# Optimization experiments

Hardware: AMD Instinct MI355X
Metric: run time of the kernel (lower is better)

The kernel has to match this reference:

```python
import math
import jax, jax.numpy as jnp
import numpy as np

V, D, H, F, L = 32128, 768, 12, 3072, 12
NUM_BUCKETS, MAX_DIST = 32, 128
B, S = 16, 512
EPS = 1e-6


def _rel_bucket(rel_pos, num_buckets=NUM_BUCKETS, max_distance=MAX_DIST):
    # bidirectional T5 bucketing
    num_buckets //= 2
    ret = (rel_pos > 0).astype(jnp.int32) * num_buckets
    n = jnp.abs(rel_pos)
    max_exact = num_buckets // 2
    is_small = n < max_exact
    large = max_exact + (
        jnp.log(n.astype(jnp.float32) / max_exact)
        / math.log(max_distance / max_exact)
        * (num_buckets - max_exact)
    ).astype(jnp.int32)
    large = jnp.minimum(large, num_buckets - 1)
    return ret + jnp.where(is_small, n.astype(jnp.int32), large)


def t5_layernorm(x, w):
    # RMS norm: no mean subtraction, no bias
    var = jnp.mean(x * x, axis=-1, keepdims=True)
    return x * jax.lax.rsqrt(var + EPS) * w


def setup_inputs() -> dict:
    key = jax.random.key(0)
    ks = jax.random.split(key, 12)
    sc = 0.02
    inp = {
        "tokens": jax.random.randint(ks[0], (B, S), 0, V, dtype=jnp.int64),
        "emb": jax.random.normal(ks[1], (V, D), jnp.float32) * sc,
        "rel_bias": jax.random.normal(ks[2], (NUM_BUCKETS, H), jnp.float32) * sc,
        "ln1_w": jnp.ones((L, D), jnp.float32),
        "wq": jax.random.normal(ks[3], (L, D, D), jnp.float32) * sc,
        "wk": jax.random.normal(ks[4], (L, D, D), jnp.float32) * sc,
        "wv": jax.random.normal(ks[5], (L, D, D), jnp.float32) * sc,
        "wo": jax.random.normal(ks[6], (L, D, D), jnp.float32) * sc,
        "ln2_w": jnp.ones((L, D), jnp.float32),
        "w1": jax.random.normal(ks[7], (L, D, F), jnp.float32) * sc,
        "w2": jax.random.normal(ks[8], (L, F, D), jnp.float32) * sc,
        "ln_final_w": jnp.ones((D,), jnp.float32),
    }
    return inp


def _attn(x, pos_bias, wq, wk, wv, wo):
    b, s, d = x.shape
    dh = d // H
    q = (x @ wq).reshape(b, s, H, dh).transpose(0, 2, 1, 3)
    k = (x @ wk).reshape(b, s, H, dh).transpose(0, 2, 1, 3)
    v = (x @ wv).reshape(b, s, H, dh).transpose(0, 2, 1, 3)
    # T5: NO 1/sqrt(dh) scaling; add bucketed relative-position bias
    scores = jnp.einsum("bhqd,bhkd->bhqk", q, k) + pos_bias[None]  # [B,H,S,S]
    a = jax.nn.softmax(scores, axis=-1)
    o = jnp.einsum("bhqk,bhkd->bhqd", a, v)
    o = o.transpose(0, 2, 1, 3).reshape(b, s, d)
    return o @ wo


def reference(tokens, emb, rel_bias, ln1_w, wq, wk, wv, wo, ln2_w, w1, w2, ln_final_w):
    x = emb[tokens]  # [B,S,D]
    s = tokens.shape[1]
    pos = jnp.arange(s)
    buckets = _rel_bucket(pos[None, :] - pos[:, None])  # [S,S]
    pos_bias = rel_bias[buckets].transpose(2, 0, 1)  # [H,S,S], computed once (layer 0)
    for i in range(L):
        h = t5_layernorm(x, ln1_w[i])
        x = x + _attn(h, pos_bias, wq[i], wk[i], wv[i], wo[i])
        h = t5_layernorm(x, ln2_w[i])
        x = x + jax.nn.relu(h @ w1[i]) @ w2[i]
    return t5_layernorm(x, ln_final_w)
```

## Files before the change

kernel.cpp:

```cpp
#include <hip/hip_runtime.h>
#include <hip/hip_bf16.h>

typedef unsigned short u16;
typedef unsigned int   u32;
typedef __attribute__((ext_vector_type(8))) __bf16 bf16x8;
typedef __attribute__((ext_vector_type(4))) float  f32x4;
typedef __attribute__((ext_vector_type(4))) u16    u16x4;

#define SEQ     512
#define DMODEL  768
#define NHEAD   12
#define DHEAD   64
#define FDIM    3072
#define NLAYER  12
#define NROWS   8192
#define QKVN    2304

__device__ __forceinline__ u16 f2bf(float f) {
  union { float f; u32 u; } x; x.f = f;
  u32 r = x.u + 0x7fffu + ((x.u >> 16) & 1u);
  return (u16)(r >> 16);
}

__global__ __launch_bounds__(256) void k_transpose_cvt(const float* __restrict__ in,
                                                       u16* __restrict__ out, int K, int N,
                                                       size_t istride, size_t ostride) {
  __shared__ float tile[32][33];
  in  += (size_t)blockIdx.z * istride;
  out += (size_t)blockIdx.z * ostride;
  int nb = blockIdx.x * 32, kb = blockIdx.y * 32;
  int tx = threadIdx.x, ty = threadIdx.y;
#pragma unroll
  for (int i = 0; i < 4; i++)
    tile[ty + 8 * i][tx] = in[(size_t)(kb + ty + 8 * i) * N + nb + tx];
  __syncthreads();
#pragma unroll
  for (int i = 0; i < 4; i++)
    out[(size_t)(nb + ty + 8 * i) * K + kb + tx] = f2bf(tile[tx][ty + 8 * i]);
}

__global__ __launch_bounds__(256) void k_embed(const int* __restrict__ tokens,
                                               const float* __restrict__ emb,
                                               float* __restrict__ x) {
  int idx = blockIdx.x * 256 + threadIdx.x;
  int row = idx / 192, c4 = idx % 192;
  int tok = tokens[row];
  reinterpret_cast<float4*>(x + (size_t)row * DMODEL)[c4] =
      reinterpret_cast<const float4*>(emb + (size_t)tok * DMODEL)[c4];
}

__global__ __launch_bounds__(256) void k_biaslut(const float* __restrict__ rel_bias,
                                                 float* __restrict__ lut) {
  int idx = blockIdx.x * 256 + threadIdx.x;
  int h = idx >> 10, i = idx & 1023;
  int rel = i - 511;
  int ret = rel > 0 ? 16 : 0;
  int n = rel < 0 ? -rel : rel;
  int b;
  if (n < 8) {
    b = n;
  } else {
    float r = logf((float)n * 0.125f) / 2.772588722239781f * 8.0f;
    int lg = 8 + (int)r;
    b = lg < 15 ? lg : 15;
  }
  b += ret;
  lut[idx] = rel_bias[b * NHEAD + h];
}

template <int BF16OUT>
__global__ __launch_bounds__(256) void k_rmsnorm(const float* __restrict__ x,
                                                 const float* __restrict__ w,
                                                 void* __restrict__ out) {
  int row = blockIdx.x * 4 + (threadIdx.x >> 6);
  int lane = threadIdx.x & 63;
  const float4* xr = reinterpret_cast<const float4*>(x + (size_t)row * DMODEL);
  float4 a = xr[lane], b = xr[lane + 64], c = xr[lane + 128];
  float ss = a.x * a.x + a.y * a.y + a.z * a.z + a.w * a.w
           + b.x * b.x + b.y * b.y + b.z * b.z + b.w * b.w
           + c.x * c.x + c.y * c.y + c.z * c.z + c.w * c.w;
#pragma unroll
  for (int off = 1; off < 64; off <<= 1) ss += __shfl_xor(ss, off);
  float sc = rsqrtf(ss * (1.0f / 768.0f) + 1e-6f);
  const float4* wr = reinterpret_cast<const float4*>(w);
  float4 w0 = wr[lane], w1 = wr[lane + 64], w2 = wr[lane + 128];
  if (BF16OUT) {
    u16x4* o = reinterpret_cast<u16x4*>((u16*)out + (size_t)row * DMODEL);
    u16x4 v0, v1, v2;
    v0[0] = f2bf(a.x * sc * w0.x); v0[1] = f2bf(a.y * sc * w0.y);
    v0[2] = f2bf(a.z * sc * w0.z); v0[3] = f2bf(a.w * sc * w0.w);
    v1[0] = f2bf(b.x * sc * w1.x); v1[1] = f2bf(b.y * sc * w1.y);
    v1[2] = f2bf(b.z * sc * w1.z); v1[3] = f2bf(b.w * sc * w1.w);
    v2[0] = f2bf(c.x * sc * w2.x); v2[1] = f2bf(c.y * sc * w2.y);
    v2[2] = f2bf(c.z * sc * w2.z); v2[3] = f2bf(c.w * sc * w2.w);
    o[lane] = v0; o[lane + 64] = v1; o[lane + 128] = v2;
  } else {
    float4* o = reinterpret_cast<float4*>((float*)out + (size_t)row * DMODEL);
    float4 v0, v1, v2;
    v0.x = a.x * sc * w0.x; v0.y = a.y * sc * w0.y; v0.z = a.z * sc * w0.z; v0.w = a.w * sc * w0.w;
    v1.x = b.x * sc * w1.x; v1.y = b.y * sc * w1.y; v1.z = b.z * sc * w1.z; v1.w = b.w * sc * w1.w;
    v2.x = c.x * sc * w2.x; v2.y = c.y * sc * w2.y; v2.z = c.z * sc * w2.z; v2.w = c.w * sc * w2.w;
    o[lane] = v0; o[lane + 64] = v1; o[lane + 128] = v2;
  }
}

__device__ __forceinline__ void gload_lds16(const void* g, void* l) {
  __builtin_amdgcn_global_load_lds((const __attribute__((address_space(1))) void*)g,
                                   (__attribute__((address_space(3))) void*)l, 16, 0, 0);
}

template <int EPI, int NF>
__global__ __launch_bounds__(512, 2) void k_gemm(const u16* __restrict__ A, const u16* __restrict__ Bt,
                                                 u16* __restrict__ outb, float* __restrict__ outf,
                                                 int M, int N, int K) {
  __shared__ u16 lds[3 * 24576];
  const int NT = K >> 6;
  const int BROWS = 2 * NF * 16;
  int tid = threadIdx.x;
  int lane = tid & 63, wid = tid >> 6;
  int lr = lane & 15, lh = lane >> 4;
  int wm = wid >> 1, wn = wid & 1;

  int gx = gridDim.x, gm = gridDim.y;
  int nwg = gx * gm;
  int linear = blockIdx.y * gx + blockIdx.x;
  int cpx = nwg >> 3;
  int swz = (linear & 7) * cpx + (linear >> 3);
  int bn = (swz % gx) * BROWS;
  int bm = (swz / gx) * 256;

  const u16* Ab = A  + (size_t)bm * K;
  const u16* Bb = Bt + (size_t)bn * K;

  f32x4 acc[4][NF] = {};

  auto STAGE_A = [&](int kt, u16* buf) {
#pragma unroll
    for (int i = 0; i < 4; i++) {
      int elem = i * 512 + tid;
      int row = elem >> 3, ch = elem & 7;
      int chs = ch ^ (row & 7);
      gload_lds16(Ab + (size_t)row * K + kt * 64 + chs * 8, buf + elem * 8);
    }
  };
  auto STAGE_B = [&](int kt, u16* buf) {
#pragma unroll
    for (int i = 0; i < 2; i++) {
      int elem = i * 512 + tid;
      int row = elem >> 3, ch = elem & 7;
      if (row >= BROWS) row = BROWS - 1;
      int chs = ch ^ (row & 7);
      gload_lds16(Bb + (size_t)row * K + kt * 64 + chs * 8, buf + 16384 + elem * 8);
    }
  };

  STAGE_A(0, lds);
  STAGE_B(0, lds);
  STAGE_A(1, lds + 24576);
  STAGE_B(1, lds + 24576);
  asm volatile("s_waitcnt vmcnt(6)" ::: "memory");
  __builtin_amdgcn_s_barrier();

  bf16x8 af[4], bfr[2][NF];

#define DSA(KK)                                                                 \
  _Pragma("unroll") for (int i = 0; i < 4; i++) {                               \
    int r = wm * 64 + i * 16 + lr;                                              \
    af[i] = *reinterpret_cast<const bf16x8*>(cur + r * 64 + ((((KK) * 4 + lh) ^ (r & 7)) * 8)); \
  }
#define MFMA_G(KK)                                                              \
  __builtin_amdgcn_s_setprio(1);                                                \
  _Pragma("unroll") for (int i = 0; i < 4; i++)                                 \
  _Pragma("unroll") for (int n = 0; n < NF; n++)                                \
    acc[i][n] = __builtin_amdgcn_mfma_f32_16x16x32_bf16(af[i], bfr[KK][n], acc[i][n], 0, 0, 0); \
  __builtin_amdgcn_s_setprio(0);
#define BAR_LGKM                                                                \
  __builtin_amdgcn_s_barrier();                                                 \
  asm volatile("s_waitcnt lgkmcnt(0)" ::: "memory");                            \
  __builtin_amdgcn_sched_barrier(0);

  int cs = 0;
  for (int t = 0; t < NT; ++t) {
    const u16* cur = lds + cs * 24576;
    int ds = cs + 2; if (ds >= 3) ds -= 3;
    u16* dst = lds + ds * 24576;
    int t2 = t + 2; if (t2 >= NT) t2 -= NT;

#pragma unroll
    for (int kk = 0; kk < 2; kk++)
#pragma unroll
      for (int n = 0; n < NF; n++) {
        int r = wn * (NF * 16) + n * 16 + lr;
        bfr[kk][n] = *reinterpret_cast<const bf16x8*>(cur + 16384 + r * 64 + (((kk * 4 + lh) ^ (r & 7)) * 8));
      }
    DSA(0)
    STAGE_A(t2, dst);
    BAR_LGKM
    MFMA_G(0)
    __builtin_amdgcn_s_barrier();

    DSA(1)
    STAGE_B(t2, dst);
    BAR_LGKM
    MFMA_G(1)
    asm volatile("s_waitcnt vmcnt(6)" ::: "memory");
    __builtin_amdgcn_s_barrier();

    cs += 1; if (cs >= 3) cs -= 3;
  }
#undef DSA
#undef MFMA_G
#undef BAR_LGKM

#pragma unroll
  for (int i = 0; i < 4; i++)
#pragma unroll
    for (int n = 0; n < NF; n++)
#pragma unroll
      for (int r = 0; r < 4; r++) {
        int row = bm + wm * 64 + i * 16 + lh * 4 + r;
        int col = bn + wn * (NF * 16) + n * 16 + lr;
        size_t idx = (size_t)row * N + col;
        float v = acc[i][n][r];
        if (EPI == 0)      outb[idx] = f2bf(v);
        else if (EPI == 1) outb[idx] = f2bf(v > 0.f ? v : 0.f);
        else               outf[idx] += v;
      }
}

__global__ __launch_bounds__(256) void k_vtrans(const u16* __restrict__ qkv, u16* __restrict__ vt) {
  __shared__ u16 t[32][33];
  int bh = blockIdx.z;
  int b = bh / NHEAD, h = bh % NHEAD;
  int d0 = blockIdx.x * 32, s0 = blockIdx.y * 32;
  int tx = threadIdx.x, ty = threadIdx.y;
  const u16* src = qkv + (size_t)(b * SEQ + s0) * QKVN + 2 * DMODEL + h * DHEAD + d0;
#pragma unroll
  for (int i = 0; i < 4; i++)
    t[ty + 8 * i][tx] = src[(size_t)(ty + 8 * i) * QKVN + tx];
  __syncthreads();
  u16* dst = vt + ((size_t)bh * DHEAD + d0) * SEQ + s0;
#pragma unroll
  for (int i = 0; i < 4; i++)
    dst[(size_t)(ty + 8 * i) * SEQ + tx] = t[tx][ty + 8 * i];
}

__global__ __launch_bounds__(256) void k_attn(const u16* __restrict__ qkv,
                                              const u16* __restrict__ vt,
                                              const float* __restrict__ lutg,
                                              u16* __restrict__ ob) {
  __shared__ __align__(16) float lut[1024];
  __shared__ __align__(16) u16 Ks[2][4096];
  __shared__ __align__(16) u16 Vs[2][4096];
  __shared__ __align__(16) u16 Ps[4][2048];
  int b = blockIdx.x / NHEAD, h = blockIdx.x % NHEAD;
  int qt = blockIdx.y;
  int tid = threadIdx.x;
  int lane = tid & 63, wid = tid >> 6;
  int lr = lane & 15, lh = lane >> 4;
  int q0 = qt * 128 + wid * 32;

  reinterpret_cast<float4*>(lut)[tid] = reinterpret_cast<const float4*>(lutg + h * 1024)[tid];

  bf16x8 aq[2][2];
#pragma unroll
  for (int m = 0; m < 2; m++) {
    const u16* qp = qkv + (size_t)(b * SEQ + q0 + m * 16 + lr) * QKVN + h * DHEAD;
#pragma unroll
    for (int kk = 0; kk < 2; kk++)
      aq[m][kk] = *reinterpret_cast<const bf16x8*>(qp + kk * 32 + lh * 8);
  }

  float mrun[2][4], lpart[2][4];
  f32x4 acc_o[2][4] = {};
#pragma unroll
  for (int m = 0; m < 2; m++)
#pragma unroll
    for (int r = 0; r < 4; r++) { mrun[m][r] = -3.0e38f; lpart[m][r] = 0.f; }

  int srow = tid >> 3, sc8 = tid & 7;
  int scs = (sc8 ^ (srow & 7)) << 3;
  const u16* kbase = qkv + (size_t)(b * SEQ + srow) * QKVN + DMODEL + h * DHEAD + scs;
  const u16* vbase = vt + ((size_t)blockIdx.x * DHEAD + srow) * SEQ + scs;

  auto STAGE = [&](int kt, int bufi) {
    int kv0 = kt << 6;
    gload_lds16(kbase + (size_t)kv0 * QKVN,        &Ks[bufi][tid * 8]);
    gload_lds16(kbase + (size_t)(kv0 + 32) * QKVN, &Ks[bufi][2048 + tid * 8]);
    gload_lds16(vbase + kv0,                       &Vs[bufi][tid * 8]);
    gload_lds16(vbase + 32 * SEQ + kv0,            &Vs[bufi][2048 + tid * 8]);
  };

  STAGE(0, 0);
  asm volatile("s_waitcnt vmcnt(0) lgkmcnt(0)" ::: "memory");
  __builtin_amdgcn_s_barrier();

  int ibase = 511 + lr - q0 - lh * 4;
  u16* pw = Ps[wid];

  for (int kt = 0; kt < 8; kt++) {
    int cb = kt & 1;
    __builtin_amdgcn_s_barrier();
    STAGE((kt + 1) & 7, cb ^ 1);
    asm volatile("s_waitcnt vmcnt(4)" ::: "memory");
    __builtin_amdgcn_s_barrier();

    const u16* KsC = Ks[cb];
    const u16* VsC = Vs[cb];
    int kv0 = kt << 6;

    f32x4 sc[2][4] = {};
#pragma unroll
    for (int kk = 0; kk < 2; kk++) {
      bf16x8 bk[4];
#pragma unroll
      for (int n = 0; n < 4; n++) {
        int row = n * 16 + lr;
        int c = (kk * 4 + lh) ^ (lr & 7);
        bk[n] = *reinterpret_cast<const bf16x8*>(KsC + row * 64 + c * 8);
      }
#pragma unroll
      for (int m = 0; m < 2; m++)
#pragma unroll
        for (int n = 0; n < 4; n++)
          sc[m][n] = __builtin_amdgcn_mfma_f32_16x16x32_bf16(aq[m][kk], bk[n], sc[m][n], 0, 0, 0);
    }

    int pred = 1;
    float vmax[2][4];
#pragma unroll
    for (int m = 0; m < 2; m++)
#pragma unroll
      for (int r = 0; r < 4; r++) {
        int ib = ibase + kv0 - m * 16 - r;
#pragma unroll
        for (int n = 0; n < 4; n++)
          sc[m][n][r] += lut[ib + n * 16];
        float v = fmaxf(fmaxf(sc[m][0][r], sc[m][1][r]), fmaxf(sc[m][2][r], sc[m][3][r]));
        v = fmaxf(v, __shfl_xor(v, 1));
        v = fmaxf(v, __shfl_xor(v, 2));
        v = fmaxf(v, __shfl_xor(v, 4));
        v = fmaxf(v, __shfl_xor(v, 8));
        vmax[m][r] = v;
        pred = pred && (v <= mrun[m][r] + 8.0f);
      }
    if (!__all(pred)) {
#pragma unroll
      for (int m = 0; m < 2; m++)
#pragma unroll
        for (int r = 0; r < 4; r++) {
          float mo = mrun[m][r];
          float mn = fmaxf(mo, vmax[m][r]);
          float corr = __expf(mo - mn);
          mrun[m][r] = mn;
          lpart[m][r] *= corr;
#pragma unroll
          for (int n = 0; n < 4; n++) acc_o[m][n][r] *= corr;
        }
    }
#pragma unroll
    for (int m = 0; m < 2; m++)
#pragma unroll
      for (int r = 0; r < 4; r++) {
        float mm = mrun[m][r];
        int prow = m * 16 + lh * 4 + r;
        int pbse = prow * 64;
        int sw = prow & 7;
        float lp = lpart[m][r];
#pragma unroll
        for (int n = 0; n < 4; n++) {
          float pv = __expf(sc[m][n][r] - mm);
          lp += pv;
          pw[pbse + ((((n << 1) | (lr >> 3)) ^ sw) << 3) + (lr & 7)] = f2bf(pv);
        }
        lpart[m][r] = lp;
      }

    asm volatile("s_waitcnt lgkmcnt(0)" ::: "memory");
    __builtin_amdgcn_sched_barrier(0);
#pragma unroll
    for (int kk = 0; kk < 2; kk++) {
      bf16x8 bvv[4], ap[2];
#pragma unroll
      for (int n = 0; n < 4; n++) {
        int row = n * 16 + lr;
        int c = (kk * 4 + lh) ^ (lr & 7);
        bvv[n] = *reinterpret_cast<const bf16x8*>(VsC + row * 64 + c * 8);
      }
#pragma unroll
      for (int m = 0; m < 2; m++) {
        int row = m * 16 + lr;
        int c = (kk * 4 + lh) ^ (lr & 7);
        ap[m] = *reinterpret_cast<const bf16x8*>(pw + row * 64 + c * 8);
      }
#pragma unroll
      for (int m = 0; m < 2; m++)
#pragma unroll
        for (int n = 0; n < 4; n++)
          acc_o[m][n] = __builtin_amdgcn_mfma_f32_16x16x32_bf16(ap[m], bvv[n], acc_o[m][n], 0, 0, 0);
    }
  }

#pragma unroll
  for (int m = 0; m < 2; m++)
#pragma unroll
    for (int r = 0; r < 4; r++) {
      float l = lpart[m][r];
      l += __shfl_xor(l, 1);
      l += __shfl_xor(l, 2);
      l += __shfl_xor(l, 4);
      l += __shfl_xor(l, 8);
      float inv = 1.f / l;
      size_t orow = (size_t)(b * SEQ + q0 + m * 16 + lh * 4 + r);
#pragma unroll
      for (int n = 0; n < 4; n++)
        ob[orow * DMODEL + h * DHEAD + n * 16 + lr] = f2bf(acc_o[m][n][r] * inv);
    }
}

extern "C" void kernel_launch(void* const* d_in, const int* in_sizes, int n_in,
                              void* d_out, int out_size, void* d_ws, size_t ws_size,
                              hipStream_t stream) {
  const int*   tokens = (const int*)  d_in[0];
  const float* emb    = (const float*)d_in[1];
  const float* relb   = (const float*)d_in[2];
  const float* ln1w   = (const float*)d_in[3];
  const float* wq     = (const float*)d_in[4];
  const float* wk     = (const float*)d_in[5];
  const float* wv     = (const float*)d_in[6];
  const float* wo     = (const float*)d_in[7];
  const float* ln2w   = (const float*)d_in[8];
  const float* w1     = (const float*)d_in[9];
  const float* w2     = (const float*)d_in[10];
  const float* lnfw   = (const float*)d_in[11];
  float* out = (float*)d_out;

  char* p = (char*)d_ws;
  auto carve = [&](size_t bytes) { char* r = p; p += (bytes + 255) & ~(size_t)255; return r; };
  const size_t DD = (size_t)DMODEL * DMODEL, DF = (size_t)DMODEL * FDIM;

  u16*   wqkv_t = (u16*)carve(NLAYER * 3 * DD * 2);
  u16*   wo_t   = (u16*)carve(NLAYER * DD * 2);
  u16*   w1_t   = (u16*)carve(NLAYER * DF * 2);
  u16*   w2_t   = (u16*)carve(NLAYER * DF * 2);
  float* x      = (float*)carve((size_t)NROWS * DMODEL * 4);
  u16*   hbuf   = (u16*)carve((size_t)NROWS * DMODEL * 2);
  u16*   qkvbuf = (u16*)carve((size_t)NROWS * QKVN * 2);
  u16*   abuf   = (u16*)carve((size_t)NROWS * DMODEL * 2);
  u16*   fbuf   = (u16*)carve((size_t)NROWS * FDIM * 2);
  float* lutbuf = (float*)carve((size_t)NHEAD * 1024 * 4);
  u16*   vtbuf  = fbuf;

  dim3 tb(32, 8);
  k_transpose_cvt<<<dim3(24, 24, NLAYER), tb, 0, stream>>>(wq, wqkv_t,          DMODEL, DMODEL, DD, 3 * DD);
  k_transpose_cvt<<<dim3(24, 24, NLAYER), tb, 0, stream>>>(wk, wqkv_t + DD,     DMODEL, DMODEL, DD, 3 * DD);
  k_transpose_cvt<<<dim3(24, 24, NLAYER), tb, 0, stream>>>(wv, wqkv_t + 2 * DD, DMODEL, DMODEL, DD, 3 * DD);
  k_transpose_cvt<<<dim3(24, 24, NLAYER), tb, 0, stream>>>(wo, wo_t,            DMODEL, DMODEL, DD, DD);
  k_transpose_cvt<<<dim3(96, 24, NLAYER), tb, 0, stream>>>(w1, w1_t,            DMODEL, FDIM,   DF, DF);
  k_transpose_cvt<<<dim3(24, 96, NLAYER), tb, 0, stream>>>(w2, w2_t,            FDIM, DMODEL,   DF, DF);

  k_embed<<<NROWS * 192 / 256, 256, 0, stream>>>(tokens, emb, x);
  k_biaslut<<<48, 256, 0, stream>>>(relb, lutbuf);

  for (int i = 0; i < NLAYER; i++) {
    k_rmsnorm<1><<<NROWS / 4, 256, 0, stream>>>(x, ln1w + i * DMODEL, hbuf);
    k_gemm<0, 3><<<dim3(24, 32), 512, 0, stream>>>(hbuf, wqkv_t + (size_t)i * 3 * DD, qkvbuf, nullptr,
                                                   NROWS, QKVN, DMODEL);
    k_vtrans<<<dim3(2, 16, 192), tb, 0, stream>>>(qkvbuf, vtbuf);
    k_attn<<<dim3(192, 4), 256, 0, stream>>>(qkvbuf, vtbuf, lutbuf, abuf);
    k_gemm<2, 3><<<dim3(8, 32),  512, 0, stream>>>(abuf, wo_t + (size_t)i * DD, nullptr, x,
                                                   NROWS, DMODEL, DMODEL);
    k_rmsnorm<1><<<NROWS / 4, 256, 0, stream>>>(x, ln2w + i * DMODEL, hbuf);
    k_gemm<1, 4><<<dim3(24, 32), 512, 0, stream>>>(hbuf, w1_t + (size_t)i * DF, fbuf, nullptr,
                                                   NROWS, FDIM, DMODEL);
    k_gemm<2, 3><<<dim3(8, 32),  512, 0, stream>>>(fbuf, w2_t + (size_t)i * DF, nullptr, x,
                                                   NROWS, DMODEL, FDIM);
  }
  k_rmsnorm<0><<<NROWS / 4, 256, 0, stream>>>(x, lnfw, out);
}
```

Before: 3.127 ms.

## Shrink GEMM tiles to 128x96 with 256 threads and double buffering

The GEMM kernel moves from 256-row tiles with 512 threads and a 3-stage LDS ring to 128x96 tiles with 256 threads and a 2-buffer ping-pong. It also drops the NF template parameter, so the FFN up-projection now uses 96-column tiles like the other GEMMs. Grids double in the M dimension to give more workgroups, smaller LDS per block and possibly higher occupancy. The cost is less operand reuse per tile and a full vmcnt(0) wait every iteration, which leaves less global-load latency hidden.

```diff
diff --git a/kernel.cpp b/kernel.cpp
--- a/kernel.cpp
+++ b/kernel.cpp
@@ -109,13 +109,12 @@
                                    (__attribute__((address_space(3))) void*)l, 16, 0, 0);
 }
 
-template <int EPI, int NF>
-__global__ __launch_bounds__(512, 2) void k_gemm(const u16* __restrict__ A, const u16* __restrict__ Bt,
+template <int EPI>
+__global__ __launch_bounds__(256, 2) void k_gemm(const u16* __restrict__ A, const u16* __restrict__ Bt,
                                                  u16* __restrict__ outb, float* __restrict__ outf,
                                                  int M, int N, int K) {
-  __shared__ u16 lds[3 * 24576];
+  __shared__ u16 lds[2 * 14336];
   const int NT = K >> 6;
-  const int BROWS = 2 * NF * 16;
   int tid = threadIdx.x;
   int lane = tid & 63, wid = tid >> 6;
   int lr = lane & 15, lh = lane >> 4;
@@ -126,18 +125,18 @@
   int linear = blockIdx.y * gx + blockIdx.x;
   int cpx = nwg >> 3;
   int swz = (linear & 7) * cpx + (linear >> 3);
-  int bn = (swz % gx) * BROWS;
-  int bm = (swz / gx) * 256;
+  int bn = (swz % gx) * 96;
+  int bm = (swz / gx) * 128;
 
   const u16* Ab = A  + (size_t)bm * K;
   const u16* Bb = Bt + (size_t)bn * K;
 
-  f32x4 acc[4][NF] = {};
+  f32x4 acc[4][3] = {};
 
   auto STAGE_A = [&](int kt, u16* buf) {
 #pragma unroll
     for (int i = 0; i < 4; i++) {
-      int elem = i * 512 + tid;
+      int elem = i * 256 + tid;
       int row = elem >> 3, ch = elem & 7;
       int chs = ch ^ (row & 7);
       gload_lds16(Ab + (size_t)row * K + kt * 64 + chs * 8, buf + elem * 8);
@@ -145,23 +144,20 @@
   };
   auto STAGE_B = [&](int kt, u16* buf) {
 #pragma unroll
-    for (int i = 0; i < 2; i++) {
-      int elem = i * 512 + tid;
+    for (int i = 0; i < 3; i++) {
+      int elem = i * 256 + tid;
       int row = elem >> 3, ch = elem & 7;
-      if (row >= BROWS) row = BROWS - 1;
       int chs = ch ^ (row & 7);
-      gload_lds16(Bb + (size_t)row * K + kt * 64 + chs * 8, buf + 16384 + elem * 8);
+      gload_lds16(Bb + (size_t)row * K + kt * 64 + chs * 8, buf + 8192 + elem * 8);
     }
   };
 
   STAGE_A(0, lds);
   STAGE_B(0, lds);
-  STAGE_A(1, lds + 24576);
-  STAGE_B(1, lds + 24576);
-  asm volatile("s_waitcnt vmcnt(6)" ::: "memory");
+  asm volatile("s_waitcnt vmcnt(0)" ::: "memory");
   __builtin_amdgcn_s_barrier();
 
-  bf16x8 af[4], bfr[2][NF];
+  bf16x8 af[4], bfr[2][3];
 
 #define DSA(KK)                                                                 \
   _Pragma("unroll") for (int i = 0; i < 4; i++) {                               \
@@ -171,7 +167,7 @@
 #define MFMA_G(KK)                                                              \
   __builtin_amdgcn_s_setprio(1);                                                \
   _Pragma("unroll") for (int i = 0; i < 4; i++)                                 \
-  _Pragma("unroll") for (int n = 0; n < NF; n++)                                \
+  _Pragma("unroll") for (int n = 0; n < 3; n++)                                 \
     acc[i][n] = __builtin_amdgcn_mfma_f32_16x16x32_bf16(af[i], bfr[KK][n], acc[i][n], 0, 0, 0); \
   __builtin_amdgcn_s_setprio(0);
 #define BAR_LGKM                                                                \
@@ -179,34 +175,30 @@
   asm volatile("s_waitcnt lgkmcnt(0)" ::: "memory");                            \
   __builtin_amdgcn_sched_barrier(0);
 
-  int cs = 0;
   for (int t = 0; t < NT; ++t) {
-    const u16* cur = lds + cs * 24576;
-    int ds = cs + 2; if (ds >= 3) ds -= 3;
-    u16* dst = lds + ds * 24576;
-    int t2 = t + 2; if (t2 >= NT) t2 -= NT;
+    const u16* cur = lds + (t & 1) * 14336;
+    u16* nxt = lds + ((t + 1) & 1) * 14336;
+    int t1 = (t + 1 < NT) ? t + 1 : 0;
 
 #pragma unroll
     for (int kk = 0; kk < 2; kk++)
 #pragma unroll
-      for (int n = 0; n < NF; n++) {
-        int r = wn * (NF * 16) + n * 16 + lr;
-        bfr[kk][n] = *reinterpret_cast<const bf16x8*>(cur + 16384 + r * 64 + (((kk * 4 + lh) ^ (r & 7)) * 8));
+      for (int n = 0; n < 3; n++) {
+        int r = wn * 48 + n * 16 + lr;
+        bfr[kk][n] = *reinterpret_cast<const bf16x8*>(cur + 8192 + r * 64 + (((kk * 4 + lh) ^ (r & 7)) * 8));
       }
     DSA(0)
-    STAGE_A(t2, dst);
+    STAGE_A(t1, nxt);
     BAR_LGKM
     MFMA_G(0)
     __builtin_amdgcn_s_barrier();
 
     DSA(1)
-    STAGE_B(t2, dst);
+    STAGE_B(t1, nxt);
     BAR_LGKM
     MFMA_G(1)
-    asm volatile("s_waitcnt vmcnt(6)" ::: "memory");
+    asm volatile("s_waitcnt vmcnt(0)" ::: "memory");
     __builtin_amdgcn_s_barrier();
-
-    cs += 1; if (cs >= 3) cs -= 3;
   }
 #undef DSA
 #undef MFMA_G
@@ -215,11 +207,11 @@
 #pragma unroll
   for (int i = 0; i < 4; i++)
 #pragma unroll
-    for (int n = 0; n < NF; n++)
+    for (int n = 0; n < 3; n++)
 #pragma unroll
       for (int r = 0; r < 4; r++) {
         int row = bm + wm * 64 + i * 16 + lh * 4 + r;
-        int col = bn + wn * (NF * 16) + n * 16 + lr;
+        int col = bn + wn * 48 + n * 16 + lr;
         size_t idx = (size_t)row * N + col;
         float v = acc[i][n][r];
         if (EPI == 0)      outb[idx] = f2bf(v);
@@ -464,17 +456,17 @@
 
   for (int i = 0; i < NLAYER; i++) {
     k_rmsnorm<1><<<NROWS / 4, 256, 0, stream>>>(x, ln1w + i * DMODEL, hbuf);
-    k_gemm<0, 3><<<dim3(24, 32), 512, 0, stream>>>(hbuf, wqkv_t + (size_t)i * 3 * DD, qkvbuf, nullptr,
-                                                   NROWS, QKVN, DMODEL);
+    k_gemm<0><<<dim3(24, 64), 256, 0, stream>>>(hbuf, wqkv_t + (size_t)i * 3 * DD, qkvbuf, nullptr,
+                                                NROWS, QKVN, DMODEL);
     k_vtrans<<<dim3(2, 16, 192), tb, 0, stream>>>(qkvbuf, vtbuf);
     k_attn<<<dim3(192, 4), 256, 0, stream>>>(qkvbuf, vtbuf, lutbuf, abuf);
-    k_gemm<2, 3><<<dim3(8, 32),  512, 0, stream>>>(abuf, wo_t + (size_t)i * DD, nullptr, x,
-                                                   NROWS, DMODEL, DMODEL);
+    k_gemm<2><<<dim3(8, 64),  256, 0, stream>>>(abuf, wo_t + (size_t)i * DD, nullptr, x,
+                                                NROWS, DMODEL, DMODEL);
     k_rmsnorm<1><<<NROWS / 4, 256, 0, stream>>>(x, ln2w + i * DMODEL, hbuf);
-    k_gemm<1, 4><<<dim3(24, 32), 512, 0, stream>>>(hbuf, w1_t + (size_t)i * DF, fbuf, nullptr,
-                                                   NROWS, FDIM, DMODEL);
-    k_gemm<2, 3><<<dim3(8, 32),  512, 0, stream>>>(fbuf, w2_t + (size_t)i * DF, nullptr, x,
-                                                   NROWS, DMODEL, FDIM);
+    k_gemm<1><<<dim3(32, 64), 256, 0, stream>>>(hbuf, w1_t + (size_t)i * DF, fbuf, nullptr,
+                                                NROWS, FDIM, DMODEL);
+    k_gemm<2><<<dim3(8, 64),  256, 0, stream>>>(fbuf, w2_t + (size_t)i * DF, nullptr, x,
+                                                NROWS, DMODEL, FDIM);
   }
   k_rmsnorm<0><<<NROWS / 4, 256, 0, stream>>>(x, lnfw, out);
 }
```

New measurement: 3.245 ms. +3.8%, slower.

## Load K/V MFMA fragments directly from global memory instead of LDS staging

Applied to the files above, without the earlier changes.

Removes the double-buffered LDS staging of K and V tiles (async global-to-LDS loads plus barriers) in the attention kernel. Each wave now reads its K and V MFMA operand fragments straight from global memory, relying on the cache for reuse across the four waves. This cuts LDS use and block-wide barriers, which may raise occupancy, but adds redundant global/L2 traffic and exposes load latency with no explicit prefetch. A __syncthreads is added after the LUT load, and the lgkmcnt wait before reading P from LDS is dropped.

```diff
diff --git a/kernel.cpp b/kernel.cpp
--- a/kernel.cpp
+++ b/kernel.cpp
@@ -250,10 +250,9 @@
                                               const float* __restrict__ lutg,
                                               u16* __restrict__ ob) {
   __shared__ __align__(16) float lut[1024];
-  __shared__ __align__(16) u16 Ks[2][4096];
-  __shared__ __align__(16) u16 Vs[2][4096];
   __shared__ __align__(16) u16 Ps[4][2048];
   int b = blockIdx.x / NHEAD, h = blockIdx.x % NHEAD;
+  int bh = blockIdx.x;
   int qt = blockIdx.y;
   int tid = threadIdx.x;
   int lane = tid & 63, wid = tid >> 6;
@@ -261,6 +260,7 @@
   int q0 = qt * 128 + wid * 32;
 
   reinterpret_cast<float4*>(lut)[tid] = reinterpret_cast<const float4*>(lutg + h * 1024)[tid];
+  __syncthreads();
 
   bf16x8 aq[2][2];
 #pragma unroll
@@ -278,35 +278,13 @@
 #pragma unroll
     for (int r = 0; r < 4; r++) { mrun[m][r] = -3.0e38f; lpart[m][r] = 0.f; }
 
-  int srow = tid >> 3, sc8 = tid & 7;
-  int scs = (sc8 ^ (srow & 7)) << 3;
-  const u16* kbase = qkv + (size_t)(b * SEQ + srow) * QKVN + DMODEL + h * DHEAD + scs;
-  const u16* vbase = vt + ((size_t)blockIdx.x * DHEAD + srow) * SEQ + scs;
-
-  auto STAGE = [&](int kt, int bufi) {
-    int kv0 = kt << 6;
-    gload_lds16(kbase + (size_t)kv0 * QKVN,        &Ks[bufi][tid * 8]);
-    gload_lds16(kbase + (size_t)(kv0 + 32) * QKVN, &Ks[bufi][2048 + tid * 8]);
-    gload_lds16(vbase + kv0,                       &Vs[bufi][tid * 8]);
-    gload_lds16(vbase + 32 * SEQ + kv0,            &Vs[bufi][2048 + tid * 8]);
-  };
-
-  STAGE(0, 0);
-  asm volatile("s_waitcnt vmcnt(0) lgkmcnt(0)" ::: "memory");
-  __builtin_amdgcn_s_barrier();
+  const u16* kfrag = qkv + (size_t)(b * SEQ + lr) * QKVN + DMODEL + h * DHEAD + lh * 8;
+  const u16* vfrag = vt + ((size_t)bh * DHEAD + lr) * SEQ + lh * 8;
 
   int ibase = 511 + lr - q0 - lh * 4;
   u16* pw = Ps[wid];
 
   for (int kt = 0; kt < 8; kt++) {
-    int cb = kt & 1;
-    __builtin_amdgcn_s_barrier();
-    STAGE((kt + 1) & 7, cb ^ 1);
-    asm volatile("s_waitcnt vmcnt(4)" ::: "memory");
-    __builtin_amdgcn_s_barrier();
-
-    const u16* KsC = Ks[cb];
-    const u16* VsC = Vs[cb];
     int kv0 = kt << 6;
 
     f32x4 sc[2][4] = {};
@@ -314,11 +292,8 @@
     for (int kk = 0; kk < 2; kk++) {
       bf16x8 bk[4];
 #pragma unroll
-      for (int n = 0; n < 4; n++) {
-        int row = n * 16 + lr;
-        int c = (kk * 4 + lh) ^ (lr & 7);
-        bk[n] = *reinterpret_cast<const bf16x8*>(KsC + row * 64 + c * 8);
-      }
+      for (int n = 0; n < 4; n++)
+        bk[n] = *reinterpret_cast<const bf16x8*>(kfrag + (size_t)(kv0 + n * 16) * QKVN + kk * 32);
 #pragma unroll
       for (int m = 0; m < 2; m++)
 #pragma unroll
@@ -376,17 +351,12 @@
         lpart[m][r] = lp;
       }
 
-    asm volatile("s_waitcnt lgkmcnt(0)" ::: "memory");
-    __builtin_amdgcn_sched_barrier(0);
 #pragma unroll
     for (int kk = 0; kk < 2; kk++) {
       bf16x8 bvv[4], ap[2];
 #pragma unroll
-      for (int n = 0; n < 4; n++) {
-        int row = n * 16 + lr;
-        int c = (kk * 4 + lh) ^ (lr & 7);
-        bvv[n] = *reinterpret_cast<const bf16x8*>(VsC + row * 64 + c * 8);
-      }
+      for (int n = 0; n < 4; n++)
+        bvv[n] = *reinterpret_cast<const bf16x8*>(vfrag + (size_t)(n * 16) * SEQ + kv0 + kk * 32);
 #pragma unroll
       for (int m = 0; m < 2; m++) {
         int row = m * 16 + lr;
```

New measurement: 3.373 ms. 7.9% more time.

## Simplify GEMM main-loop schedule to one barrier per k-tile and prioritize attention MFMAs

Applied to the files above, without the earlier changes.

The GEMM main loop now issues both A and B global-to-LDS stages at the top of each k-tile, then does the LDS reads and MFMAs for the two k-halves with no intermediate barriers. Only one barrier plus vmcnt wait is kept per iteration, and B fragments are held for one k-half at a time. This is meant to cut barrier and lgkmcnt stalls and register pressure in the triple-buffered pipeline, but leaves the compiler to interleave ds_reads with MFMAs without explicit waits. The attention kernel also wraps its QK and PV MFMA blocks in s_setprio raises so those waves win issue arbitration.

```diff
diff --git a/kernel.cpp b/kernel.cpp
--- a/kernel.cpp
+++ b/kernel.cpp
@@ -160,24 +160,26 @@
   STAGE_B(1, lds + 24576);
   asm volatile("s_waitcnt vmcnt(6)" ::: "memory");
   __builtin_amdgcn_s_barrier();
-
-  bf16x8 af[4], bfr[2][NF];
+  __builtin_amdgcn_sched_barrier(0);
+
+  bf16x8 af[4], bfr[NF];
 
 #define DSA(KK)                                                                 \
   _Pragma("unroll") for (int i = 0; i < 4; i++) {                               \
     int r = wm * 64 + i * 16 + lr;                                              \
     af[i] = *reinterpret_cast<const bf16x8*>(cur + r * 64 + ((((KK) * 4 + lh) ^ (r & 7)) * 8)); \
   }
-#define MFMA_G(KK)                                                              \
+#define DSB(KK)                                                                 \
+  _Pragma("unroll") for (int n = 0; n < NF; n++) {                              \
+    int r = wn * (NF * 16) + n * 16 + lr;                                       \
+    bfr[n] = *reinterpret_cast<const bf16x8*>(cur + 16384 + r * 64 + ((((KK) * 4 + lh) ^ (r & 7)) * 8)); \
+  }
+#define MFMA_G                                                                  \
   __builtin_amdgcn_s_setprio(1);                                                \
   _Pragma("unroll") for (int i = 0; i < 4; i++)                                 \
   _Pragma("unroll") for (int n = 0; n < NF; n++)                                \
-    acc[i][n] = __builtin_amdgcn_mfma_f32_16x16x32_bf16(af[i], bfr[KK][n], acc[i][n], 0, 0, 0); \
+    acc[i][n] = __builtin_amdgcn_mfma_f32_16x16x32_bf16(af[i], bfr[n], acc[i][n], 0, 0, 0); \
   __builtin_amdgcn_s_setprio(0);
-#define BAR_LGKM                                                                \
-  __builtin_amdgcn_s_barrier();                                                 \
-  asm volatile("s_waitcnt lgkmcnt(0)" ::: "memory");                            \
-  __builtin_amdgcn_sched_barrier(0);
 
   int cs = 0;
   for (int t = 0; t < NT; ++t) {
@@ -186,31 +188,26 @@
     u16* dst = lds + ds * 24576;
     int t2 = t + 2; if (t2 >= NT) t2 -= NT;
 
-#pragma unroll
-    for (int kk = 0; kk < 2; kk++)
-#pragma unroll
-      for (int n = 0; n < NF; n++) {
-        int r = wn * (NF * 16) + n * 16 + lr;
-        bfr[kk][n] = *reinterpret_cast<const bf16x8*>(cur + 16384 + r * 64 + (((kk * 4 + lh) ^ (r & 7)) * 8));
-      }
+    STAGE_A(t2, dst);
+    STAGE_B(t2, dst);
+
+    DSB(0)
     DSA(0)
-    STAGE_A(t2, dst);
-    BAR_LGKM
-    MFMA_G(0)
-    __builtin_amdgcn_s_barrier();
-
+    MFMA_G
+
+    DSB(1)
     DSA(1)
-    STAGE_B(t2, dst);
-    BAR_LGKM
-    MFMA_G(1)
+    MFMA_G
+
     asm volatile("s_waitcnt vmcnt(6)" ::: "memory");
     __builtin_amdgcn_s_barrier();
+    __builtin_amdgcn_sched_barrier(0);
 
     cs += 1; if (cs >= 3) cs -= 3;
   }
 #undef DSA
+#undef DSB
 #undef MFMA_G
-#undef BAR_LGKM
 
 #pragma unroll
   for (int i = 0; i < 4; i++)
@@ -319,11 +316,13 @@
         int c = (kk * 4 + lh) ^ (lr & 7);
         bk[n] = *reinterpret_cast<const bf16x8*>(KsC + row * 64 + c * 8);
       }
+      __builtin_amdgcn_s_setprio(1);
 #pragma unroll
       for (int m = 0; m < 2; m++)
 #pragma unroll
         for (int n = 0; n < 4; n++)
           sc[m][n] = __builtin_amdgcn_mfma_f32_16x16x32_bf16(aq[m][kk], bk[n], sc[m][n], 0, 0, 0);
+      __builtin_amdgcn_s_setprio(0);
     }
 
     int pred = 1;
@@ -393,11 +392,13 @@
         int c = (kk * 4 + lh) ^ (lr & 7);
         ap[m] = *reinterpret_cast<const bf16x8*>(pw + row * 64 + c * 8);
       }
+      __builtin_amdgcn_s_setprio(1);
 #pragma unroll
       for (int m = 0; m < 2; m++)
 #pragma unroll
         for (int n = 0; n < 4; n++)
           acc_o[m][n] = __builtin_amdgcn_mfma_f32_16x16x32_bf16(ap[m], bvv[n], acc_o[m][n], 0, 0, 0);
+      __builtin_amdgcn_s_setprio(0);
     }
   }
 
```

Result: no change. 3.170 ms (+1.4%).
